# Performance work log

Measured on AMD Instinct MI355X. Metric: run time of the kernel, lower is better.

Reference implementation:

```python
import jax, jax.numpy as jnp
import numpy as np

N = 50000
E = 800000
H = 8
DH = 32  # hidden 256 / heads 8


def gat_layer(h, src, dst, W, a_src, a_dst, b):
    # h: [N, 256] -> per-head projected features [N, H, DH]
    hp = (h @ W).reshape(N, H, DH)
    # per-node attention logits for src/dst roles: [N, H]
    s_src = jnp.einsum('nhd,hd->nh', hp, a_src)
    s_dst = jnp.einsum('nhd,hd->nh', hp, a_dst)
    e = jax.nn.leaky_relu(s_src[src] + s_dst[dst], negative_slope=0.2)  # [Et, H]
    # segment softmax over incoming edges of each dst node
    m = jax.ops.segment_max(e, dst, num_segments=N)  # [N, H]
    ex = jnp.exp(e - m[dst])
    denom = jax.ops.segment_sum(ex, dst, num_segments=N)  # [N, H] (>0: self-loops)
    alpha = ex / denom[dst]  # [Et, H]
    out = jax.ops.segment_sum(alpha[:, :, None] * hp[src], dst, num_segments=N)
    return out.reshape(N, H * DH) + b


def han_forward(x, edges, proj_W, proj_b, gat_W, gat_asrc, gat_adst, gat_b,
                sem_W1, sem_b1, sem_W2, cls_W1, cls_b1, cls_W2, cls_b2):
    h0 = x @ proj_W + proj_b  # [N, 256]
    loop = jnp.arange(N, dtype=edges.dtype)
    embs = []
    for p in range(edges.shape[0]):  # 3 meta-paths (fixed, small)
        src = jnp.concatenate([edges[p, 0], loop])  # add self-loops (PyG default)
        dst = jnp.concatenate([edges[p, 1], loop])
        h = h0
        for l in range(2):  # 2 GAT layers per meta-path
            h = gat_layer(h, src, dst, gat_W[p, l], gat_asrc[p, l], gat_adst[p, l], gat_b[p, l])
            h = jax.nn.elu(h)  # dropout: eval-mode no-op
        embs.append(h)
    emb = jnp.stack(embs, axis=1)  # [N, P, 256]
    scores = (jnp.tanh(emb @ sem_W1 + sem_b1) @ sem_W2).squeeze(-1)  # [N, P]
    w = jax.nn.softmax(scores, axis=1)
    z = jnp.sum(emb * w[:, :, None], axis=1)  # [N, 256]
    hcls = jax.nn.relu(z @ cls_W1 + cls_b1)
    logits = hcls @ cls_W2 + cls_b2  # [N, 2]
    return logits


def setup_inputs() -> dict:
    key = jax.random.key(0)
    ks = jax.random.split(key, 16)
    s = 0.05
    return {
        'x': jax.random.normal(ks[0], (N, 128), jnp.float32),
        'edges': jax.random.randint(ks[1], (3, 2, E), 0, N, dtype=jnp.int32),
        'proj_W': jax.random.normal(ks[2], (128, 256), jnp.float32) * s,
        'proj_b': jnp.zeros((256,), jnp.float32),
        'gat_W': jax.random.normal(ks[3], (3, 2, 256, 256), jnp.float32) * s,
        'gat_asrc': jax.random.normal(ks[4], (3, 2, H, DH), jnp.float32) * s,
        'gat_adst': jax.random.normal(ks[5], (3, 2, H, DH), jnp.float32) * s,
        'gat_b': jnp.zeros((3, 2, 256), jnp.float32),
        'sem_W1': jax.random.normal(ks[6], (256, 128), jnp.float32) * s,
        'sem_b1': jnp.zeros((128,), jnp.float32),
        'sem_W2': jax.random.normal(ks[7], (128, 1), jnp.float32) * s,
        'cls_W1': jax.random.normal(ks[8], (256, 128), jnp.float32) * s,
        'cls_b1': jnp.zeros((128,), jnp.float32),
        'cls_W2': jax.random.normal(ks[9], (128, 2), jnp.float32) * s,
        'cls_b2': jnp.zeros((2,), jnp.float32),
    }


def reference(x, edges, proj_W, proj_b, gat_W, gat_asrc, gat_adst, gat_b,
              sem_W1, sem_b1, sem_W2, cls_W1, cls_b1, cls_W2, cls_b2):
    return han_forward(x, edges, proj_W, proj_b, gat_W, gat_asrc, gat_adst, gat_b,
                       sem_W1, sem_b1, sem_W2, cls_W1, cls_b1, cls_W2, cls_b2)
```

## Files before the change

kernel.cpp:

```cpp
#include <hip/hip_runtime.h>
#include <hip/hip_fp16.h>
#include <math.h>

#define N_NODES 50000
#define N_EDG   800000
#define NH      8
#define DH      32
#define HID     256
#define MAXD    64
#define FILLB   98
#define EPB     4096

typedef __attribute__((ext_vector_type(8))) short bf16x8;
typedef __attribute__((ext_vector_type(4))) float f32x4;

__device__ __forceinline__ unsigned short f2bf(float x) {
    unsigned u = __float_as_uint(x);
    u += 0x7FFF + ((u >> 16) & 1);
    return (unsigned short)(u >> 16);
}
__device__ __forceinline__ float bf2f(unsigned short h) {
    return __uint_as_float(((unsigned)h) << 16);
}
__device__ __forceinline__ float fastrcp(float x) {
    float r;
    asm("v_rcp_f32 %0, %1" : "=v"(r) : "v"(x));
    return r;
}
__device__ __forceinline__ void split8(const float4& a, const float4& b,
                                       uint4& hi, uint4& lo) {
    float v[8] = {a.x,a.y,a.z,a.w,b.x,b.y,b.z,b.w};
    unsigned short h[8], l[8];
    #pragma unroll
    for (int i = 0; i < 8; ++i) { h[i] = f2bf(v[i]); l[i] = f2bf(v[i] - bf2f(h[i])); }
    hi = make_uint4(h[0]|((unsigned)h[1]<<16), h[2]|((unsigned)h[3]<<16),
                    h[4]|((unsigned)h[5]<<16), h[6]|((unsigned)h[7]<<16));
    lo = make_uint4(l[0]|((unsigned)l[1]<<16), l[2]|((unsigned)l[3]<<16),
                    l[4]|((unsigned)l[5]<<16), l[6]|((unsigned)l[7]<<16));
}
__device__ __forceinline__ void h8_to_pair(uint4 r, uint4& hi, uint4& lo) {
    const __half2* hp = (const __half2*)&r;
    unsigned short h[8], l[8];
    #pragma unroll
    for (int i = 0; i < 4; ++i) {
        float2 f = __half22float2(hp[i]);
        h[2*i]   = f2bf(f.x); l[2*i]   = f2bf(f.x - bf2f(h[2*i]));
        h[2*i+1] = f2bf(f.y); l[2*i+1] = f2bf(f.y - bf2f(h[2*i+1]));
    }
    hi = make_uint4(h[0]|((unsigned)h[1]<<16), h[2]|((unsigned)h[3]<<16),
                    h[4]|((unsigned)h[5]<<16), h[6]|((unsigned)h[7]<<16));
    lo = make_uint4(l[0]|((unsigned)l[1]<<16), l[2]|((unsigned)l[3]<<16),
                    l[4]|((unsigned)l[5]<<16), l[6]|((unsigned)l[7]<<16));
}

__device__ __forceinline__ void fmix2(float& alo, float& ahi, unsigned rv, float w) {
    asm("v_fma_mix_f32 %0, %1, %2, %0 op_sel:[0,0,0] op_sel_hi:[1,0,0]"
        : "+v"(alo) : "v"(rv), "v"(w));
    asm("v_fma_mix_f32 %0, %1, %2, %0 op_sel:[1,0,0] op_sel_hi:[1,0,0]"
        : "+v"(ahi) : "v"(rv), "v"(w));
}

template<int NC, int ACT, int OUTMODE, int AMODE>
__global__ __launch_bounds__(256)
void mfma_gemm_k(const float* __restrict__ A32p, const __half* __restrict__ A16p,
                 int lda,
                 const unsigned short* __restrict__ WThi,
                 const unsigned short* __restrict__ WTlo,
                 const float* __restrict__ bias,
                 float* __restrict__ C, __half* __restrict__ Ch,
                 int ldc, int M, int K) {
    __shared__ unsigned short sAh[128*32], sAl[128*32], sBh[128*32], sBl[128*32];
    const int tid  = threadIdx.x;
    const int lane = tid & 63;
    const int w    = tid >> 6;
    const int wr   = w >> 1, wc = w & 1;
    const int r0   = blockIdx.x * 128;
    const int c0   = blockIdx.y * 128;
    const int l15  = lane & 15, q = lane >> 4;

    const int cl8   = (((lane & 3) ^ ((lane >> 4) & 3)) << 3);
    const int lrow  = w*32 + (lane >> 2);
    const int gbrow0 = c0 + lrow, gbrow1 = c0 + lrow + 16;
    const int lbase = w * 1024;
    const int ldst  = lbase + lane * 8;

    const int srow = tid >> 2, slot = tid & 3;
    const size_t ga0 = (size_t)min(r0 + srow,      M - 1) * lda + slot * 8;
    const size_t ga1 = (size_t)min(r0 + srow + 64, M - 1) * lda + slot * 8;
    const int lda0 = srow*32 + ((slot ^ ((srow >> 2) & 3)) << 3);
    const int lda1 = lda0 + 64*32;

    f32x4 acc[4][4];
    #pragma unroll
    for (int i = 0; i < 4; ++i)
        #pragma unroll
        for (int j = 0; j < 4; ++j) acc[i][j] = (f32x4){0.f, 0.f, 0.f, 0.f};

    const int swzF = (l15 >> 2) & 3;
    const int qs   = ((q ^ swzF) << 3);

    const int nsteps = K >> 5;
    for (int s = 0; s < nsteps; ++s) {
        const int kc = s << 5;
        __syncthreads();
        uint4 h0, l0, h1, l1;
        if constexpr (AMODE == 0) {
            float4 f0a = *(const float4*)&A32p[ga0 + kc];
            float4 f0b = *(const float4*)&A32p[ga0 + kc + 4];
            float4 f1a = *(const float4*)&A32p[ga1 + kc];
            float4 f1b = *(const float4*)&A32p[ga1 + kc + 4];
            split8(f0a, f0b, h0, l0);
            split8(f1a, f1b, h1, l1);
        } else {
            uint4 r0v = *(const uint4*)&A16p[ga0 + kc];
            uint4 r1v = *(const uint4*)&A16p[ga1 + kc];
            h8_to_pair(r0v, h0, l0);
            h8_to_pair(r1v, h1, l1);
        }
        *(uint4*)&sAh[lda0] = h0; *(uint4*)&sAl[lda0] = l0;
        *(uint4*)&sAh[lda1] = h1; *(uint4*)&sAl[lda1] = l1;
        *(uint4*)&sBh[ldst]       = *(const uint4*)&WThi[(size_t)gbrow0*K + kc + cl8];
        *(uint4*)&sBh[ldst + 512] = *(const uint4*)&WThi[(size_t)gbrow1*K + kc + cl8];
        *(uint4*)&sBl[ldst]       = *(const uint4*)&WTlo[(size_t)gbrow0*K + kc + cl8];
        *(uint4*)&sBl[ldst + 512] = *(const uint4*)&WTlo[(size_t)gbrow1*K + kc + cl8];
        __syncthreads();

        bf16x8 fAh[4], fAl[4];
        #pragma unroll
        for (int t = 0; t < 4; ++t) {
            int ra = (wr*64 + t*16 + l15) * 32 + qs;
            fAh[t] = *(const bf16x8*)&sAh[ra];
            fAl[t] = *(const bf16x8*)&sAl[ra];
        }
        #pragma unroll
        for (int nt = 0; nt < 4; ++nt) {
            int rb = (wc*64 + nt*16 + l15) * 32 + qs;
            bf16x8 fBh = *(const bf16x8*)&sBh[rb];
            bf16x8 fBl = *(const bf16x8*)&sBl[rb];
            #pragma unroll
            for (int mt = 0; mt < 4; ++mt) {
                acc[mt][nt] = __builtin_amdgcn_mfma_f32_16x16x32_bf16(fAh[mt], fBh, acc[mt][nt], 0, 0, 0);
                acc[mt][nt] = __builtin_amdgcn_mfma_f32_16x16x32_bf16(fAh[mt], fBl, acc[mt][nt], 0, 0, 0);
                acc[mt][nt] = __builtin_amdgcn_mfma_f32_16x16x32_bf16(fAl[mt], fBh, acc[mt][nt], 0, 0, 0);
            }
        }
    }
    #pragma unroll
    for (int mt = 0; mt < 4; ++mt)
        #pragma unroll
        for (int nt = 0; nt < 4; ++nt) {
            int col = c0 + wc*64 + nt*16 + l15;
            float bb = bias ? bias[col] : 0.f;
            #pragma unroll
            for (int r = 0; r < 4; ++r) {
                int grow = r0 + wr*64 + mt*16 + q*4 + r;
                if (grow < M) {
                    float v = acc[mt][nt][r] + bb;
                    if (ACT == 1) {
                        float t = __expf(2.f * v);
                        v = 1.f - 2.f * fastrcp(1.f + t);
                    } else if (ACT == 2) v = fmaxf(v, 0.f);
                    size_t o = (size_t)grow * ldc + col;
                    if (OUTMODE == 2) Ch[o] = __float2half(v);
                    else              C[o] = v;
                }
            }
        }
}

template<int FILL>
__global__ __launch_bounds__(256)
void mfma_gemm3_k(const __half* __restrict__ A16p, int aoffz, int lda,
                  const unsigned short* __restrict__ WT, int l,
                  __half* __restrict__ hp3, int M,
                  const int* __restrict__ edges, int* __restrict__ cnt3,
                  unsigned short* __restrict__ slots3) {
    __shared__ unsigned short sAh[128*32], sAl[128*32], sBh[128*32], sBl[128*32];
    const int gx = (M + 127) >> 7;
    if constexpr (FILL) {
        if ((int)blockIdx.x >= gx) {
            const int fb = ((int)blockIdx.x - gx) + FILLB * (blockIdx.y + 2 * blockIdx.z);
            const int base = fb * EPB + threadIdx.x;
            #pragma unroll 1
            for (int t = 0; t < 4; ++t) {
                int dd[4], ss[4];
                #pragma unroll
                for (int j = 0; j < 4; ++j) {
                    int e = base + (t * 4 + j) * 256;
                    if (e < 3 * N_EDG) {
                        int p = e / N_EDG, i = e - p * N_EDG;
                        const int* src = edges + (size_t)p * 2 * N_EDG;
                        int s = src[i], d = src[N_EDG + i];
                        ss[j] = min(max(s, 0), N_NODES - 1);
                        dd[j] = p * N_NODES + min(max(d, 0), N_NODES - 1);
                    } else { ss[j] = -1; dd[j] = 0; }
                }
                int pos[4];
                #pragma unroll
                for (int j = 0; j < 4; ++j)
                    if (ss[j] >= 0) pos[j] = atomicAdd(&cnt3[dd[j]], 1);
                #pragma unroll
                for (int j = 0; j < 4; ++j)
                    if (ss[j] >= 0 && pos[j] < MAXD)
                        slots3[(size_t)dd[j] * MAXD + pos[j]] = (unsigned short)ss[j];
            }
            return;
        }
    }
    const int p = blockIdx.z;
    A16p += (size_t)p * aoffz;
    const unsigned short* WThi = WT + (size_t)(2*p + l) * 131072;
    const unsigned short* WTlo = WThi + 65536;
    __half* Ch = hp3 + (size_t)p * N_NODES * HID;
    const int K = HID;

    const int tid  = threadIdx.x;
    const int lane = tid & 63;
    const int w    = tid >> 6;
    const int wr   = w >> 1, wc = w & 1;
    const int r0   = blockIdx.x * 128;
    const int c0   = blockIdx.y * 128;
    const int l15  = lane & 15, q = lane >> 4;

    const int cl8   = (((lane & 3) ^ ((lane >> 4) & 3)) << 3);
    const int lrow  = w*32 + (lane >> 2);
    const int gbrow0 = c0 + lrow, gbrow1 = c0 + lrow + 16;
    const int lbase = w * 1024;
    const int ldst  = lbase + lane * 8;

    const int srow = tid >> 2, slot = tid & 3;
    const size_t ga0 = (size_t)min(r0 + srow,      M - 1) * lda + slot * 8;
    const size_t ga1 = (size_t)min(r0 + srow + 64, M - 1) * lda + slot * 8;
    const int lda0 = srow*32 + ((slot ^ ((srow >> 2) & 3)) << 3);
    const int lda1 = lda0 + 64*32;

    f32x4 acc[4][4];
    #pragma unroll
    for (int i = 0; i < 4; ++i)
        #pragma unroll
        for (int j = 0; j < 4; ++j) acc[i][j] = (f32x4){0.f, 0.f, 0.f, 0.f};

    const int swzF = (l15 >> 2) & 3;
    const int qs   = ((q ^ swzF) << 3);

    for (int s = 0; s < 8; ++s) {
        const int kc = s << 5;
        __syncthreads();
        uint4 r0v = *(const uint4*)&A16p[ga0 + kc];
        uint4 r1v = *(const uint4*)&A16p[ga1 + kc];
        uint4 h0, l0, h1, l1;
        h8_to_pair(r0v, h0, l0);
        h8_to_pair(r1v, h1, l1);
        *(uint4*)&sAh[lda0] = h0; *(uint4*)&sAl[lda0] = l0;
        *(uint4*)&sAh[lda1] = h1; *(uint4*)&sAl[lda1] = l1;
        *(uint4*)&sBh[ldst]       = *(const uint4*)&WThi[(size_t)gbrow0*K + kc + cl8];
        *(uint4*)&sBh[ldst + 512] = *(const uint4*)&WThi[(size_t)gbrow1*K + kc + cl8];
        *(uint4*)&sBl[ldst]       = *(const uint4*)&WTlo[(size_t)gbrow0*K + kc + cl8];
        *(uint4*)&sBl[ldst + 512] = *(const uint4*)&WTlo[(size_t)gbrow1*K + kc + cl8];
        __syncthreads();

        bf16x8 fAh[4], fAl[4];
        #pragma unroll
        for (int t = 0; t < 4; ++t) {
            int ra = (wr*64 + t*16 + l15) * 32 + qs;
            fAh[t] = *(const bf16x8*)&sAh[ra];
            fAl[t] = *(const bf16x8*)&sAl[ra];
        }
        #pragma unroll
        for (int nt = 0; nt < 4; ++nt) {
            int rb = (wc*64 + nt*16 + l15) * 32 + qs;
            bf16x8 fBh = *(const bf16x8*)&sBh[rb];
            bf16x8 fBl = *(const bf16x8*)&sBl[rb];
            #pragma unroll
            for (int mt = 0; mt < 4; ++mt) {
                acc[mt][nt] = __builtin_amdgcn_mfma_f32_16x16x32_bf16(fAh[mt], fBh, acc[mt][nt], 0, 0, 0);
                acc[mt][nt] = __builtin_amdgcn_mfma_f32_16x16x32_bf16(fAh[mt], fBl, acc[mt][nt], 0, 0, 0);
                acc[mt][nt] = __builtin_amdgcn_mfma_f32_16x16x32_bf16(fAl[mt], fBh, acc[mt][nt], 0, 0, 0);
            }
        }
    }
    #pragma unroll
    for (int mt = 0; mt < 4; ++mt)
        #pragma unroll
        for (int nt = 0; nt < 4; ++nt) {
            int col = c0 + wc*64 + nt*16 + l15;
            #pragma unroll
            for (int r = 0; r < 4; ++r) {
                int grow = r0 + wr*64 + mt*16 + q*4 + r;
                if (grow < M)
                    Ch[(size_t)grow * HID + col] = __float2half(acc[mt][nt][r]);
            }
        }
}

__global__ __launch_bounds__(256)
void cvtWall_k(const float* __restrict__ gatW, const float* __restrict__ projW,
               const float* __restrict__ semW1, const float* __restrict__ clsW1,
               unsigned short* __restrict__ WT) {
    int y = blockIdx.y;
    const float* W; int K, N;
    if (y < 6)       { W = gatW + (size_t)y * 65536; K = 256; N = 256; }
    else if (y == 6) { W = projW; K = 128; N = 256; }
    else if (y == 7) { W = semW1; K = 256; N = 128; }
    else             { W = clsW1; K = 256; N = 128; }
    int idx = blockIdx.x * 256 + threadIdx.x;
    if (idx >= K * N) return;
    unsigned short* hi = WT + (size_t)y * 131072;
    unsigned short* lo = hi + 65536;
    int k = idx / N, n = idx - k * N;
    float v = W[idx];
    unsigned short h = f2bf(v);
    hi[n * K + k] = h;
    lo[n * K + k] = f2bf(v - bf2f(h));
}

__global__ __launch_bounds__(256)
void attn_scores3_k(const __half* __restrict__ hp3,
                    const float* __restrict__ gatAs, const float* __restrict__ gatAd,
                    int l, float* __restrict__ ssrc3, float* __restrict__ sdst3) {
    int p = blockIdx.y;
    int gid = blockIdx.x * 256 + threadIdx.x;
    if (gid >= N_NODES * NH) return;
    int h = gid & 7;
    const __half2* hv = (const __half2*)(hp3 + (size_t)p * N_NODES * HID + (size_t)gid * DH);
    const float* a = gatAs + (2*p + l) * HID + h * DH;
    const float* d = gatAd + (2*p + l) * HID + h * DH;
    float ss = 0.f, sd = 0.f;
    #pragma unroll
    for (int j = 0; j < 8; ++j) {
        float4 av = ((const float4*)a)[j], dv = ((const float4*)d)[j];
        float2 f0 = __half22float2(hv[2*j]);
        float2 f1 = __half22float2(hv[2*j + 1]);
        ss += f0.x*av.x + f0.y*av.y + f1.x*av.z + f1.y*av.w;
        sd += f0.x*dv.x + f0.y*dv.y + f1.x*dv.z + f1.y*dv.w;
    }
    ssrc3[p * N_NODES * NH + gid] = ss;
    sdst3[p * N_NODES * NH + gid] = sd;
}

__global__ __launch_bounds__(256)
void zero_k(int* p, int n) { int i = blockIdx.x*256 + threadIdx.x; if (i < n) p[i] = 0; }

__global__ __launch_bounds__(256)
void agg3_k(const int* __restrict__ cnt3, const unsigned short* __restrict__ slots3,
            const float* __restrict__ ssrc3, const float* __restrict__ sdst3,
            const __half* __restrict__ hp3, const float* __restrict__ gatB, int l,
            __half* __restrict__ emb16) {
    const int p = blockIdx.y;
    int wid  = (blockIdx.x * blockDim.x + threadIdx.x) >> 6;
    int lane = threadIdx.x & 63;
    if (wid >= N_NODES) return;
    const int n = wid;
    const unsigned short* srcs = slots3 + ((size_t)p * N_NODES + n) * MAXD;
    const float* s_src = ssrc3 + p * N_NODES * NH;
    const float* s_dst = sdst3 + p * N_NODES * NH;
    const __half* hp = hp3 + (size_t)p * N_NODES * HID;
    const float* bias = gatB + (2*p + l) * HID;
    const int deg = min(cnt3[p * N_NODES + n], MAXD);

    const int sub = lane & 31, eo = lane >> 5;
    const int h2  = sub >> 2;
    const float sd2 = s_dst[n*NH + h2];
    const uint4* hp4 = (const uint4*)hp;
    float dn = 0.f;
    float a0=0.f,a1=0.f,a2=0.f,a3=0.f,a4=0.f,a5=0.f,a6=0.f,a7=0.f;

    int i = eo;
    for (; i + 6 < deg; i += 8) {
        const int s0 = srcs[i];
        const int s1 = srcs[i + 2];
        const int s2 = srcs[i + 4];
        const int s3 = srcs[i + 6];
        const float x0 = s_src[s0*NH + h2];
        const float x1 = s_src[s1*NH + h2];
        const float x2 = s_src[s2*NH + h2];
        const float x3 = s_src[s3*NH + h2];
        const uint4 r0 = hp4[s0*32 + sub];
        const uint4 r1 = hp4[s1*32 + sub];
        const uint4 r2 = hp4[s2*32 + sub];
        const uint4 r3 = hp4[s3*32 + sub];
        float e0 = x0 + sd2; e0 = e0 > 0.f ? e0 : 0.2f * e0;
        float e1 = x1 + sd2; e1 = e1 > 0.f ? e1 : 0.2f * e1;
        float e2 = x2 + sd2; e2 = e2 > 0.f ? e2 : 0.2f * e2;
        float e3 = x3 + sd2; e3 = e3 > 0.f ? e3 : 0.2f * e3;
        const float w0 = __expf(e0), w1 = __expf(e1);
        const float w2 = __expf(e2), w3 = __expf(e3);
        dn += w0; dn += w1; dn += w2; dn += w3;
        fmix2(a0, a1, r0.x, w0); fmix2(a2, a3, r0.y, w0);
        fmix2(a4, a5, r0.z, w0); fmix2(a6, a7, r0.w, w0);
        fmix2(a0, a1, r1.x, w1); fmix2(a2, a3, r1.y, w1);
        fmix2(a4, a5, r1.z, w1); fmix2(a6, a7, r1.w, w1);
        fmix2(a0, a1, r2.x, w2); fmix2(a2, a3, r2.y, w2);
        fmix2(a4, a5, r2.z, w2); fmix2(a6, a7, r2.w, w2);
        fmix2(a0, a1, r3.x, w3); fmix2(a2, a3, r3.y, w3);
        fmix2(a4, a5, r3.z, w3); fmix2(a6, a7, r3.w, w3);
    }
    for (; i + 2 < deg; i += 4) {
        const int s0 = srcs[i];
        const int s1 = srcs[i + 2];
        const float x0 = s_src[s0*NH + h2];
        const float x1 = s_src[s1*NH + h2];
        const uint4 r0 = hp4[s0*32 + sub];
        const uint4 r1 = hp4[s1*32 + sub];
        float e0 = x0 + sd2; e0 = e0 > 0.f ? e0 : 0.2f * e0;
        float e1 = x1 + sd2; e1 = e1 > 0.f ? e1 : 0.2f * e1;
        const float w0 = __expf(e0), w1 = __expf(e1);
        dn += w0; dn += w1;
        fmix2(a0, a1, r0.x, w0); fmix2(a2, a3, r0.y, w0);
        fmix2(a4, a5, r0.z, w0); fmix2(a6, a7, r0.w, w0);
        fmix2(a0, a1, r1.x, w1); fmix2(a2, a3, r1.y, w1);
        fmix2(a4, a5, r1.z, w1); fmix2(a6, a7, r1.w, w1);
    }
    if (i < deg) {
        const int s0 = srcs[i];
        const float x0 = s_src[s0*NH + h2];
        const uint4 r0 = hp4[s0*32 + sub];
        float e0 = x0 + sd2; e0 = e0 > 0.f ? e0 : 0.2f * e0;
        const float w0 = __expf(e0);
        dn += w0;
        fmix2(a0, a1, r0.x, w0); fmix2(a2, a3, r0.y, w0);
        fmix2(a4, a5, r0.z, w0); fmix2(a6, a7, r0.w, w0);
    }
    dn += __shfl_xor(dn, 32);
    a0 += __shfl_xor(a0, 32); a1 += __shfl_xor(a1, 32);
    a2 += __shfl_xor(a2, 32); a3 += __shfl_xor(a3, 32);
    a4 += __shfl_xor(a4, 32); a5 += __shfl_xor(a5, 32);
    a6 += __shfl_xor(a6, 32); a7 += __shfl_xor(a7, 32);
    if (lane < 32) {
        float evs = s_src[n*NH + h2] + sd2;
        evs = evs > 0.f ? evs : 0.2f * evs;
        float ws = __expf(evs);
        dn += ws;
        const uint4 rs = hp4[n*32 + sub];
        fmix2(a0, a1, rs.x, ws); fmix2(a2, a3, rs.y, ws);
        fmix2(a4, a5, rs.z, ws); fmix2(a6, a7, rs.w, ws);

        float rdn = fastrcp(dn);
        float v[8] = {a0,a1,a2,a3,a4,a5,a6,a7};
        const float4 b0 = *(const float4*)&bias[sub*8];
        const float4 b1 = *(const float4*)&bias[sub*8 + 4];
        v[0]=v[0]*rdn+b0.x; v[1]=v[1]*rdn+b0.y; v[2]=v[2]*rdn+b0.z; v[3]=v[3]*rdn+b0.w;
        v[4]=v[4]*rdn+b1.x; v[5]=v[5]*rdn+b1.y; v[6]=v[6]*rdn+b1.z; v[7]=v[7]*rdn+b1.w;
        unsigned short hh[8];
        #pragma unroll
        for (int k = 0; k < 8; ++k) {
            float e = v[k] > 0.f ? v[k] : (__expf(v[k]) - 1.f);
            hh[k] = __half_as_ushort(__float2half(e));
        }
        size_t o = (size_t)n * 768 + p * HID + sub * 8;
        *(uint4*)&emb16[o] = make_uint4(hh[0]|((unsigned)hh[1]<<16), hh[2]|((unsigned)hh[3]<<16),
                                        hh[4]|((unsigned)hh[5]<<16), hh[6]|((unsigned)hh[7]<<16));
    }
}

__global__ __launch_bounds__(256)
void score_z_k(const float* t, const float* __restrict__ W2,
               const __half* __restrict__ emb16, float* z) {
    int wid  = (blockIdx.x * blockDim.x + threadIdx.x) >> 6;
    int lane = threadIdx.x & 63;
    if (wid >= N_NODES) return;
    const int n = wid;
    float sc[3];
    #pragma unroll
    for (int p = 0; p < 3; ++p) {
        const float* tr = t + (size_t)(n*3 + p) * 128;
        float part = tr[lane] * W2[lane] + tr[64 + lane] * W2[64 + lane];
        #pragma unroll
        for (int o = 1; o < 64; o <<= 1) part += __shfl_xor(part, o);
        sc[p] = part;
    }
    float m  = fmaxf(sc[0], fmaxf(sc[1], sc[2]));
    float e0 = __expf(sc[0]-m), e1 = __expf(sc[1]-m), e2 = __expf(sc[2]-m);
    float rs = fastrcp(e0 + e1 + e2);
    e0 *= rs; e1 *= rs; e2 *= rs;
    const __half* er = emb16 + (size_t)n * 768;
    for (int c = lane; c < 256; c += 64) {
        float v0 = __half2float(er[c]);
        float v1 = __half2float(er[256 + c]);
        float v2 = __half2float(er[512 + c]);
        z[(size_t)n*384 + c] = e0*v0 + e1*v1 + e2*v2;
    }
}

__global__ __launch_bounds__(256)
void logits_k(const float* __restrict__ hcls, const float* __restrict__ W2,
              const float* __restrict__ b2, float* __restrict__ out) {
    int gid = blockIdx.x*256 + threadIdx.x;
    if (gid >= N_NODES * 2) return;
    int n = gid >> 1, o = gid & 1;
    const float* hr = hcls + (size_t)n * 128;
    float a = b2[o];
    #pragma unroll 4
    for (int j = 0; j < 128; ++j) a += hr[j] * W2[j*2 + o];
    out[gid] = a;
}

extern "C" void kernel_launch(void* const* d_in, const int* in_sizes, int n_in,
                              void* d_out, int out_size, void* d_ws, size_t ws_size,
                              hipStream_t stream) {
    (void)in_sizes; (void)n_in; (void)out_size; (void)ws_size;
    const float* x     = (const float*)d_in[0];
    const int*   edges = (const int*)  d_in[1];
    const float* projW = (const float*)d_in[2];
    const float* projb = (const float*)d_in[3];
    const float* gatW  = (const float*)d_in[4];
    const float* gatAs = (const float*)d_in[5];
    const float* gatAd = (const float*)d_in[6];
    const float* gatB  = (const float*)d_in[7];
    const float* semW1 = (const float*)d_in[8];
    const float* semb1 = (const float*)d_in[9];
    const float* semW2 = (const float*)d_in[10];
    const float* clsW1 = (const float*)d_in[11];
    const float* clsb1 = (const float*)d_in[12];
    const float* clsW2 = (const float*)d_in[13];
    const float* clsb2 = (const float*)d_in[14];
    float* out = (float*)d_out;

    char* base = (char*)d_ws;
    const size_t PLANE = (size_t)N_NODES * HID * 2;
    __half* hp3   = (__half*)(base);
    __half* emb16 = (__half*)(base + 3*PLANE);
    __half* h016  = (__half*)(base + 6*PLANE);
    char* small = base + 7*PLANE;
    float* ssrc3 = (float*)small;
    float* sdst3 = ssrc3 + 3*(size_t)N_NODES*NH;
    int*   cnt3  = (int*)(sdst3 + 3*(size_t)N_NODES*NH);
    unsigned short* WT = (unsigned short*)(cnt3 + 3*N_NODES);
    unsigned short* slots3 = WT + 9*131072;
    float* tbuf = (float*)base;
    float* hcls = (float*)(base + 6*PLANE);

    dim3 blk(256);
    const int gx = (N_NODES + 127) / 128;

    cvtWall_k<<<dim3(256, 9), blk, 0, stream>>>(gatW, projW, semW1, clsW1, WT);
    zero_k  <<<(3*N_NODES+255)/256, blk, 0, stream>>>(cnt3, 3*N_NODES);

    mfma_gemm_k<256,0,2,0><<<dim3(gx,2), blk, 0, stream>>>(
        x, nullptr, 128, WT + 6*131072, WT + 6*131072 + 65536, projb,
        nullptr, h016, 256, N_NODES, 128);

    for (int l = 0; l < 2; ++l) {
        if (l == 0)
            mfma_gemm3_k<1><<<dim3(gx + FILLB, 2, 3), blk, 0, stream>>>(
                h016, 0, HID, WT, 0, hp3, N_NODES, edges, cnt3, slots3);
        else
            mfma_gemm3_k<0><<<dim3(gx, 2, 3), blk, 0, stream>>>(
                emb16, HID, 3*HID, WT, 1, hp3, N_NODES, edges, cnt3, slots3);
        attn_scores3_k<<<dim3((N_NODES*NH+255)/256, 3), blk, 0, stream>>>(
            hp3, gatAs, gatAd, l, ssrc3, sdst3);
        agg3_k<<<dim3((N_NODES*64)/256, 3), blk, 0, stream>>>(
            cnt3, slots3, ssrc3, sdst3, hp3, gatB, l, emb16);
    }

    mfma_gemm_k<128,1,0,1><<<dim3((150000+127)/128, 1), blk, 0, stream>>>(
        nullptr, emb16, 256, WT + 7*131072, WT + 7*131072 + 65536, semb1,
        tbuf, nullptr, 128, 150000, 256);
    score_z_k<<<(N_NODES*64)/256, blk, 0, stream>>>(tbuf, semW2, emb16, tbuf);
    mfma_gemm_k<128,2,0,0><<<dim3(gx, 1), blk, 0, stream>>>(
        tbuf, nullptr, 384, WT + 8*131072, WT + 8*131072 + 65536, clsb1,
        hcls, nullptr, 128, N_NODES, 256);
    logits_k<<<(N_NODES*2+255)/256, blk, 0, stream>>>(hcls, clsW2, clsb2, out);
}
```

Measured before the change: 984.7 us.

## Split edge-bucketing fill between projection GEMM and first GAT GEMM launches

Moves part of the edge bucketing (atomic counting and slot writes) into extra blocks of the input projection GEMM launch, leaving the rest in the first-layer batched GEMM. The aim is to balance the side work across two GEMM launches so it overlaps with more matrix work and shortens the gemm3 tail. The fill helper is factored out and the GEMM template gains a FILL parameter, which adds block-count constants that must cover every edge exactly.

```diff
diff --git a/kernel.cpp b/kernel.cpp
--- a/kernel.cpp
+++ b/kernel.cpp
@@ -8,8 +8,10 @@
 #define DH      32
 #define HID     256
 #define MAXD    64
-#define FILLB   98
 #define EPB     4096
+#define PROJ_FB 88
+#define PROJ_EB (176*EPB)
+#define G3_FB   69
 
 typedef __attribute__((ext_vector_type(8))) short bf16x8;
 typedef __attribute__((ext_vector_type(4))) float f32x4;
@@ -60,7 +62,37 @@
         : "+v"(ahi) : "v"(rv), "v"(w));
 }
 
-template<int NC, int ACT, int OUTMODE, int AMODE>
+__device__ __forceinline__ void fill_edges(const int* __restrict__ edges,
+                                           int* __restrict__ cnt3,
+                                           unsigned short* __restrict__ slots3,
+                                           int fb, int ebase) {
+    const int base = ebase + fb * EPB + (int)threadIdx.x;
+    #pragma unroll 1
+    for (int t = 0; t < 4; ++t) {
+        int dd[4], ss[4];
+        #pragma unroll
+        for (int j = 0; j < 4; ++j) {
+            int e = base + (t * 4 + j) * 256;
+            if (e < 3 * N_EDG) {
+                int p = e / N_EDG, i = e - p * N_EDG;
+                const int* src = edges + (size_t)p * 2 * N_EDG;
+                int s = src[i], d = src[N_EDG + i];
+                ss[j] = min(max(s, 0), N_NODES - 1);
+                dd[j] = p * N_NODES + min(max(d, 0), N_NODES - 1);
+            } else { ss[j] = -1; dd[j] = 0; }
+        }
+        int pos[4];
+        #pragma unroll
+        for (int j = 0; j < 4; ++j)
+            if (ss[j] >= 0) pos[j] = atomicAdd(&cnt3[dd[j]], 1);
+        #pragma unroll
+        for (int j = 0; j < 4; ++j)
+            if (ss[j] >= 0 && pos[j] < MAXD)
+                slots3[(size_t)dd[j] * MAXD + pos[j]] = (unsigned short)ss[j];
+    }
+}
+
+template<int NC, int ACT, int OUTMODE, int AMODE, int FILL>
 __global__ __launch_bounds__(256)
 void mfma_gemm_k(const float* __restrict__ A32p, const __half* __restrict__ A16p,
                  int lda,
@@ -68,8 +100,18 @@
                  const unsigned short* __restrict__ WTlo,
                  const float* __restrict__ bias,
                  float* __restrict__ C, __half* __restrict__ Ch,
-                 int ldc, int M, int K) {
+                 int ldc, int M, int K,
+                 const int* __restrict__ edges, int* __restrict__ cnt3,
+                 unsigned short* __restrict__ slots3) {
     __shared__ unsigned short sAh[128*32], sAl[128*32], sBh[128*32], sBl[128*32];
+    if constexpr (FILL) {
+        const int gxk = (M + 127) >> 7;
+        if ((int)blockIdx.x >= gxk) {
+            fill_edges(edges, cnt3, slots3,
+                       ((int)blockIdx.x - gxk) + PROJ_FB * (int)blockIdx.y, 0);
+            return;
+        }
+    }
     const int tid  = threadIdx.x;
     const int lane = tid & 63;
     const int w    = tid >> 6;
@@ -179,31 +221,9 @@
     const int gx = (M + 127) >> 7;
     if constexpr (FILL) {
         if ((int)blockIdx.x >= gx) {
-            const int fb = ((int)blockIdx.x - gx) + FILLB * (blockIdx.y + 2 * blockIdx.z);
-            const int base = fb * EPB + threadIdx.x;
-            #pragma unroll 1
-            for (int t = 0; t < 4; ++t) {
-                int dd[4], ss[4];
-                #pragma unroll
-                for (int j = 0; j < 4; ++j) {
-                    int e = base + (t * 4 + j) * 256;
-                    if (e < 3 * N_EDG) {
-                        int p = e / N_EDG, i = e - p * N_EDG;
-                        const int* src = edges + (size_t)p * 2 * N_EDG;
-                        int s = src[i], d = src[N_EDG + i];
-                        ss[j] = min(max(s, 0), N_NODES - 1);
-                        dd[j] = p * N_NODES + min(max(d, 0), N_NODES - 1);
-                    } else { ss[j] = -1; dd[j] = 0; }
-                }
-                int pos[4];
-                #pragma unroll
-                for (int j = 0; j < 4; ++j)
-                    if (ss[j] >= 0) pos[j] = atomicAdd(&cnt3[dd[j]], 1);
-                #pragma unroll
-                for (int j = 0; j < 4; ++j)
-                    if (ss[j] >= 0 && pos[j] < MAXD)
-                        slots3[(size_t)dd[j] * MAXD + pos[j]] = (unsigned short)ss[j];
-            }
+            fill_edges(edges, cnt3, slots3,
+                       ((int)blockIdx.x - gx) + G3_FB * ((int)blockIdx.y + 2 * (int)blockIdx.z),
+                       PROJ_EB);
             return;
         }
     }
@@ -536,13 +556,13 @@
     cvtWall_k<<<dim3(256, 9), blk, 0, stream>>>(gatW, projW, semW1, clsW1, WT);
     zero_k  <<<(3*N_NODES+255)/256, blk, 0, stream>>>(cnt3, 3*N_NODES);
 
-    mfma_gemm_k<256,0,2,0><<<dim3(gx,2), blk, 0, stream>>>(
+    mfma_gemm_k<256,0,2,0,1><<<dim3(gx + PROJ_FB, 2), blk, 0, stream>>>(
         x, nullptr, 128, WT + 6*131072, WT + 6*131072 + 65536, projb,
-        nullptr, h016, 256, N_NODES, 128);
+        nullptr, h016, 256, N_NODES, 128, edges, cnt3, slots3);
 
     for (int l = 0; l < 2; ++l) {
         if (l == 0)
-            mfma_gemm3_k<1><<<dim3(gx + FILLB, 2, 3), blk, 0, stream>>>(
+            mfma_gemm3_k<1><<<dim3(gx + G3_FB, 2, 3), blk, 0, stream>>>(
                 h016, 0, HID, WT, 0, hp3, N_NODES, edges, cnt3, slots3);
         else
             mfma_gemm3_k<0><<<dim3(gx, 2, 3), blk, 0, stream>>>(
@@ -553,12 +573,12 @@
             cnt3, slots3, ssrc3, sdst3, hp3, gatB, l, emb16);
     }
 
-    mfma_gemm_k<128,1,0,1><<<dim3((150000+127)/128, 1), blk, 0, stream>>>(
+    mfma_gemm_k<128,1,0,1,0><<<dim3((150000+127)/128, 1), blk, 0, stream>>>(
         nullptr, emb16, 256, WT + 7*131072, WT + 7*131072 + 65536, semb1,
-        tbuf, nullptr, 128, 150000, 256);
+        tbuf, nullptr, 128, 150000, 256, nullptr, nullptr, nullptr);
     score_z_k<<<(N_NODES*64)/256, blk, 0, stream>>>(tbuf, semW2, emb16, tbuf);
-    mfma_gemm_k<128,2,0,0><<<dim3(gx, 1), blk, 0, stream>>>(
+    mfma_gemm_k<128,2,0,0,0><<<dim3(gx, 1), blk, 0, stream>>>(
         tbuf, nullptr, 384, WT + 8*131072, WT + 8*131072 + 65536, clsb1,
-        hcls, nullptr, 128, N_NODES, 256);
+        hcls, nullptr, 128, N_NODES, 256, nullptr, nullptr, nullptr);
     logits_k<<<(N_NODES*2+255)/256, blk, 0, stream>>>(hcls, clsW2, clsb2, out);
 }
```

Result: no change. 984.2 us (-0.1%).
